# Kernel optimization log

Measured on AMD Instinct MI355X. Metric: run time of the kernel, lower is better.

The kernel has to match this reference:

```python
import jax, jax.numpy as jnp
import numpy as np

B, T, D = 4, 4096, 1024
EPS = 1e-5  # FusedRMSNormSwishGate default eps


def setup_inputs() -> dict:
    key = jax.random.key(0)
    ks = jax.random.split(key, 6)
    s = 1.0 / np.sqrt(D)
    return {
        "x": jax.random.normal(ks[0], (B, T, D), jnp.float32),
        "Wi": jax.random.normal(ks[1], (D, D), jnp.float32) * s,
        "Wf": jax.random.normal(ks[2], (D, D), jnp.float32) * s,
        "Wg": jax.random.normal(ks[3], (D, D), jnp.float32) * s,
        "Wo": jax.random.normal(ks[4], (D, D), jnp.float32) * s,
        "norm_w": jnp.ones((D,), jnp.float32),
    }


def _hgrn_scan(f, i):
    # h_t = f_t * h_{t-1} + i_t  (elementwise gated linear recurrence)
    # associative combine: (f1,i1) o (f2,i2) = (f1*f2, i1*f2 + i2)
    def combine(a, b):
        fa, ia = a
        fb, ib = b
        return fa * fb, ia * fb + ib

    _, h = jax.lax.associative_scan(combine, (f, i), axis=1)
    return h


def reference(x, Wi, Wf, Wg, Wo, norm_w):
    # projections
    i = x @ Wi.T                                  # [B,T,D]
    f = jax.nn.sigmoid(x @ Wf.T)                  # forget gate in (0,1)
    # swiglu(i, 1-f): silu on the value, gated by the input gate (1-f)
    inp = jax.nn.silu(i) * (1.0 - f)
    # hierarchically-gated linear recurrence (chunk/parallel scan form)
    h = _hgrn_scan(f, inp)                        # [B,T,D]
    # RMSNorm(h) * swish(g) output gate
    g = x @ Wg.T
    rms = h * jax.lax.rsqrt(jnp.mean(h * h, axis=-1, keepdims=True) + EPS)
    o = (rms * norm_w) * (g * jax.nn.sigmoid(g))
    return o @ Wo.T
```

## Files before the change

kernel.cpp:

```cpp
#include <hip/hip_runtime.h>
#include <hip/hip_bf16.h>

typedef unsigned short u16;
using bf16x8 = __bf16 __attribute__((ext_vector_type(8)));
using f32x4  = float  __attribute__((ext_vector_type(4)));

#define BB 4
#define TT 4096
#define DD 1024
#define MROWS (BB*TT)
#define CT 64
#define NC (TT/CT)

__device__ __forceinline__ float sigm(float x) { return 1.0f / (1.0f + __expf(-x)); }
__device__ __forceinline__ u16 f2bf(float f) {
    __hip_bfloat16 h = __float2bfloat16(f);
    return *reinterpret_cast<u16*>(&h);
}
__device__ __forceinline__ float bf2f(u16 u) { return __uint_as_float(((unsigned)u) << 16); }

__device__ __forceinline__ void async_cp16(const u16* g, u16* l) {
    __builtin_amdgcn_global_load_lds(
        (const __attribute__((address_space(1))) unsigned int*)g,
        (__attribute__((address_space(3))) unsigned int*)l, 16, 0, 0);
}

__global__ __launch_bounds__(256) void conv_x_kernel(const float* __restrict__ s,
                                                     u16* __restrict__ d) {
    size_t i = (size_t)blockIdx.x * 256 + threadIdx.x;
    float4 v = *(const float4*)(s + i * 4);
    ushort4 u;
    u.x = f2bf(v.x); u.y = f2bf(v.y); u.z = f2bf(v.z); u.w = f2bf(v.w);
    *(ushort4*)(d + i * 4) = u;
}

__global__ __launch_bounds__(256) void conv_w4_kernel(const float* __restrict__ w0,
                                                      const float* __restrict__ w1,
                                                      const float* __restrict__ w2,
                                                      const float* __restrict__ w3,
                                                      u16* __restrict__ dst) {
    int i = blockIdx.x * 256 + threadIdx.x;
    int sel = i >> 18;
    int off = i & 262143;
    const float* s = (sel == 0) ? w0 : (sel == 1) ? w1 : (sel == 2) ? w2 : w3;
    float4 v = *(const float4*)(s + (size_t)off * 4);
    ushort4 u;
    u.x = f2bf(v.x); u.y = f2bf(v.y); u.z = f2bf(v.z); u.w = f2bf(v.w);
    *(ushort4*)(dst + ((size_t)sel << 20) + (size_t)off * 4) = u;
}

#define G_BM 256
#define G_BN 256
#define G_BK 64

#define READ_A(dst, MH)                                                         \
  { const u16* Ab = &As[(p * 2 + (MH)) << 13];                                  \
    _Pragma("unroll") for (int kk = 0; kk < 2; kk++) {                          \
      const int gsw = (((kk * 4 + lq) ^ lr7) << 3);                             \
      _Pragma("unroll") for (int f = 0; f < 4; f++)                             \
        dst[f][kk] = *(const bf16x8*)(Ab + (wm * 64 + f * 16 + lr) * 64 + gsw); \
    } }
#define READ_B(dst, NH)                                                         \
  { const u16* Bb = &Bs[(p * 2 + (NH)) << 13];                                  \
    _Pragma("unroll") for (int kk = 0; kk < 2; kk++) {                          \
      const int gsw = (((kk * 4 + lq) ^ lr7) << 3);                             \
      _Pragma("unroll") for (int j = 0; j < 2; j++)                             \
        dst[j][kk] = *(const bf16x8*)(Bb + (wn * 32 + j * 16 + lr) * 64 + gsw); \
    } }
#define MFMA16(AV, BV, MH, NH)                                                  \
  { _Pragma("unroll") for (int kk = 0; kk < 2; kk++)                            \
    _Pragma("unroll") for (int f = 0; f < 4; f++)                               \
    _Pragma("unroll") for (int j = 0; j < 2; j++)                               \
      acc[(MH)*4+f][(NH)*2+j] = __builtin_amdgcn_mfma_f32_16x16x32_bf16(        \
          AV[f][kk], BV[j][kk], acc[(MH)*4+f][(NH)*2+j], 0, 0, 0); }
#define SYNC_PRE()                                                              \
  do { __builtin_amdgcn_s_barrier();                                            \
       asm volatile("s_waitcnt lgkmcnt(0)" ::: "memory");                       \
       __builtin_amdgcn_s_setprio(1); } while (0)
#define SYNC_POST()                                                             \
  do { __builtin_amdgcn_s_setprio(0);                                           \
       __builtin_amdgcn_s_barrier(); } while (0)

template <typename OutT>
__global__ __launch_bounds__(512, 2)
void gemm256(const u16* __restrict__ Ag, const u16* __restrict__ Bg, int K,
             OutT* __restrict__ P0, OutT* __restrict__ P1, OutT* __restrict__ P2) {
    __shared__ u16 As[32768];
    __shared__ u16 Bs[32768];

    const int tid  = threadIdx.x;
    const int lane = tid & 63;
    const int wid  = tid >> 6;
    const int wm   = wid >> 2;
    const int wn   = wid & 3;
    const int lr   = lane & 15;
    const int lq   = lane >> 4;
    const int lr7  = lr & 7;

    const long bM  = (long)blockIdx.y * G_BM;
    const long bN0 = (long)blockIdx.x * G_BN;
    const int  KT  = K >> 6;

    auto stageA = [&](int cc, int h) {
#pragma unroll
        for (int l = 0; l < 2; l++) {
            const int G  = l * 512 + tid;
            const int rl = G >> 3;
            const int gk = (G & 7) ^ (rl & 7);
            const int r  = (rl & 63) + h * 64 + ((rl >> 6) << 7);
            async_cp16(Ag + (bM + r) * K + cc * 64 + gk * 8,
                       &As[(((cc & 1) * 2 + h) << 13) + G * 8]);
        }
    };
    auto stageB = [&](int cc, int h) {
#pragma unroll
        for (int l = 0; l < 2; l++) {
            const int G  = l * 512 + tid;
            const int rl = G >> 3;
            const int gk = (G & 7) ^ (rl & 7);
            const int r  = (rl & 31) + h * 32 + ((rl >> 5) << 6);
            async_cp16(Bg + (bN0 + r) * K + cc * 64 + gk * 8,
                       &Bs[(((cc & 1) * 2 + h) << 13) + G * 8]);
        }
    };

    const f32x4 zero = {0.f, 0.f, 0.f, 0.f};
    f32x4 acc[8][4];
#pragma unroll
    for (int i = 0; i < 8; i++)
#pragma unroll
        for (int j = 0; j < 4; j++) acc[i][j] = zero;

    stageA(0, 0); stageB(0, 0); stageA(0, 1); stageB(0, 1);
    if (KT > 1) {
        stageA(1, 0); stageB(1, 0);
        asm volatile("s_waitcnt vmcnt(4)" ::: "memory");
    } else {
        asm volatile("s_waitcnt vmcnt(0)" ::: "memory");
    }
    __builtin_amdgcn_s_barrier();

    for (int c = 0; c < KT; ++c) {
        const int  p  = c & 1;
        const bool s1 = (c + 1 < KT);
        const bool s2 = (c + 2 < KT);
        bf16x8 av0[4][2], av1[4][2], bv0[2][2], bv1[2][2];
        READ_A(av0, 0); READ_B(bv0, 0);
        if (s1) stageA(c + 1, 1);
        SYNC_PRE(); MFMA16(av0, bv0, 0, 0); SYNC_POST();
        READ_B(bv1, 1);
        if (s1) stageB(c + 1, 1);
        SYNC_PRE(); MFMA16(av0, bv1, 0, 1); SYNC_POST();
        READ_A(av1, 1);
        if (s2) stageA(c + 2, 0);
        SYNC_PRE(); MFMA16(av1, bv0, 1, 0); SYNC_POST();
        if (s2) {
            stageB(c + 2, 0);
            asm volatile("s_waitcnt vmcnt(4)" ::: "memory");
        } else if (s1) {
            asm volatile("s_waitcnt vmcnt(0)" ::: "memory");
        }
        SYNC_PRE(); MFMA16(av1, bv1, 1, 1); SYNC_POST();
    }

    const int pl = (int)(bN0 >> 10);
    OutT* P = (pl == 0) ? P0 : ((pl == 1) ? P1 : P2);
    const int cn = (int)(bN0 & 1023);
#pragma unroll
    for (int i = 0; i < 8; i++) {
        const long m0 = bM + wm * 128 + i * 16 + lq * 4;
#pragma unroll
        for (int j = 0; j < 4; j++) {
            const int n = cn + wn * 64 + j * 16 + lr;
#pragma unroll
            for (int r = 0; r < 4; r++) {
                if constexpr (sizeof(OutT) == 2)
                    P[(m0 + r) * 1024 + n] = f2bf(acc[i][j][r]);
                else
                    P[(m0 + r) * 1024 + n] = acc[i][j][r];
            }
        }
    }
}

__global__ __launch_bounds__(256) void scan_pass1(const u16* __restrict__ ip,
                                                  const u16* __restrict__ fp,
                                                  float* __restrict__ Fc,
                                                  float* __restrict__ Ic) {
    const int tid = blockIdx.x * 256 + threadIdx.x;
    const int d4  = tid & 255;
    const int c   = (tid >> 8) & (NC - 1);
    const int b   = tid >> 14;
    size_t base = ((size_t)(b * TT + c * CT) << 10) + (size_t)d4 * 4;
    float F[4] = {1.f, 1.f, 1.f, 1.f};
    float I[4] = {0.f, 0.f, 0.f, 0.f};
#pragma unroll 8
    for (int t = 0; t < CT; t++) {
        ushort4 fu = *(const ushort4*)(fp + base);
        ushort4 iu = *(const ushort4*)(ip + base);
        base += DD;
        const u16 fa[4] = {fu.x, fu.y, fu.z, fu.w};
        const u16 ia[4] = {iu.x, iu.y, iu.z, iu.w};
#pragma unroll
        for (int j = 0; j < 4; j++) {
            float f  = sigm(bf2f(fa[j]));
            float iv = bf2f(ia[j]);
            float v  = iv * sigm(iv) * (1.f - f);
            I[j] = fmaf(f, I[j], v);
            F[j] *= f;
        }
    }
    const size_t o = (((size_t)(b * NC + c)) << 10) + (size_t)d4 * 4;
    float4 vF = {F[0], F[1], F[2], F[3]};
    float4 vI = {I[0], I[1], I[2], I[3]};
    *(float4*)(Fc + o) = vF;
    *(float4*)(Ic + o) = vI;
}

__global__ __launch_bounds__(256) void scan_pass2(const float* __restrict__ Fc,
                                                  const float* __restrict__ Ic,
                                                  float* __restrict__ Hin) {
    const int gtid = blockIdx.x * 256 + threadIdx.x;
    const int lane = gtid & 63;
    const int w    = gtid >> 6;
    const int b    = w >> 10;
    const int d    = w & 1023;
    const int idx  = ((b * NC + lane) << 10) + d;
    float F = Fc[idx];
    float I = Ic[idx];
#pragma unroll
    for (int s = 1; s < 64; s <<= 1) {
        float Fp = __shfl_up(F, s, 64);
        float Ip = __shfl_up(I, s, 64);
        if (lane >= s) {
            I = fmaf(Ip, F, I);
            F *= Fp;
        }
    }
    float Hex = __shfl_up(I, 1, 64);
    if (lane == 0) Hex = 0.f;
    Hin[idx] = Hex;
}

__global__ __launch_bounds__(256) void scan_pass3(const u16* __restrict__ ip,
                                                  const u16* __restrict__ fp,
                                                  const float* __restrict__ Hin,
                                                  u16* __restrict__ hout) {
    const int tid = blockIdx.x * 256 + threadIdx.x;
    const int d4  = tid & 255;
    const int c   = (tid >> 8) & (NC - 1);
    const int b   = tid >> 14;
    size_t base = ((size_t)(b * TT + c * CT) << 10) + (size_t)d4 * 4;
    const size_t o = (((size_t)(b * NC + c)) << 10) + (size_t)d4 * 4;
    float4 hv = *(const float4*)(Hin + o);
    float h[4] = {hv.x, hv.y, hv.z, hv.w};
#pragma unroll 8
    for (int t = 0; t < CT; t++) {
        ushort4 fu = *(const ushort4*)(fp + base);
        ushort4 iu = *(const ushort4*)(ip + base);
        const u16 fa[4] = {fu.x, fu.y, fu.z, fu.w};
        const u16 ia[4] = {iu.x, iu.y, iu.z, iu.w};
        ushort4 ou;
        u16 oa[4];
#pragma unroll
        for (int j = 0; j < 4; j++) {
            float f  = sigm(bf2f(fa[j]));
            float iv = bf2f(ia[j]);
            float v  = iv * sigm(iv) * (1.f - f);
            h[j] = fmaf(f, h[j], v);
            oa[j] = f2bf(h[j]);
        }
        ou.x = oa[0]; ou.y = oa[1]; ou.z = oa[2]; ou.w = oa[3];
        *(ushort4*)(hout + base) = ou;
        base += DD;
    }
}

__global__ __launch_bounds__(256) void rmsnorm_gate(const u16* hin,
                                                    const u16* __restrict__ g,
                                                    const float* __restrict__ w,
                                                    u16* oout) {
    const int row = blockIdx.x;
    const int t = threadIdx.x;
    const size_t base = ((size_t)row << 10) + t * 4;
    ushort4 hu = *(const ushort4*)(hin + base);
    float h0 = bf2f(hu.x), h1 = bf2f(hu.y), h2 = bf2f(hu.z), h3 = bf2f(hu.w);
    float ss = h0 * h0 + h1 * h1 + h2 * h2 + h3 * h3;
#pragma unroll
    for (int o = 32; o > 0; o >>= 1) ss += __shfl_down(ss, o);
    __shared__ float red[4];
    if ((t & 63) == 0) red[t >> 6] = ss;
    __syncthreads();
    const float tot = red[0] + red[1] + red[2] + red[3];
    const float rms = rsqrtf(tot * (1.f / 1024.f) + 1e-5f);
    ushort4 gu = *(const ushort4*)(g + base);
    float g0 = bf2f(gu.x), g1 = bf2f(gu.y), g2 = bf2f(gu.z), g3 = bf2f(gu.w);
    float4 wv = *(const float4*)(w + (size_t)t * 4);
    ushort4 ou;
    ou.x = f2bf(h0 * rms * wv.x * g0 * sigm(g0));
    ou.y = f2bf(h1 * rms * wv.y * g1 * sigm(g1));
    ou.z = f2bf(h2 * rms * wv.z * g2 * sigm(g2));
    ou.w = f2bf(h3 * rms * wv.w * g3 * sigm(g3));
    *(ushort4*)(oout + base) = ou;
}

extern "C" void kernel_launch(void* const* d_in, const int* in_sizes, int n_in,
                              void* d_out, int out_size, void* d_ws, size_t ws_size,
                              hipStream_t stream) {
    const float* x  = (const float*)d_in[0];
    const float* Wi = (const float*)d_in[1];
    const float* Wf = (const float*)d_in[2];
    const float* Wg = (const float*)d_in[3];
    const float* Wo = (const float*)d_in[4];
    const float* nw = (const float*)d_in[5];
    float* out = (float*)d_out;

    const size_t MB = 1ull << 20;
    char* ws = (char*)d_ws;
    u16*   xo  = (u16*)(ws);
    u16*   Wb  = (u16*)(ws + 32 * MB);
    u16*   Pi  = (u16*)(ws + 40 * MB);
    u16*   Pf  = (u16*)(ws + 72 * MB);
    float* Fc  = (float*)(ws + 104 * MB);
    float* Ic  = Fc + BB * NC * DD;
    float* Hin = Ic + BB * NC * DD;
    u16*   g   = (u16*)d_out;

    conv_x_kernel<<<16384, 256, 0, stream>>>(x, xo);
    conv_w4_kernel<<<4096, 256, 0, stream>>>(Wi, Wf, Wg, Wo, Wb);
    gemm256<u16><<<dim3(12, 64), 512, 0, stream>>>(xo, Wb, 1024, Pi, Pf, g);
    scan_pass1<<<256, 256, 0, stream>>>(Pi, Pf, Fc, Ic);
    scan_pass2<<<1024, 256, 0, stream>>>(Fc, Ic, Hin);
    scan_pass3<<<256, 256, 0, stream>>>(Pi, Pf, Hin, xo);
    rmsnorm_gate<<<16384, 256, 0, stream>>>(xo, g, nw, xo);
    gemm256<float><<<dim3(4, 64), 512, 0, stream>>>(xo, Wb + 3ull * 1024 * 1024, 1024,
                                                    out, out, out);
}
```

Baseline: 382.2 us.

## Use inline-asm LDS reads in big GEMM and smaller-tile GEMM for output projection

The fused QKV-style 256x256 GEMM now reads LDS through inline ds_read_b128 with immediate offsets and adds a sched_barrier so the compiler cannot reorder them around the sync points. The final output projection switches to a new, simpler 128x128-tile kernel with 256 threads, launched on 1024 blocks instead of 256. The aim is to cut LDS address arithmetic and to fill more CUs on the small final GEMM. The trade-off is that the new kernel is single-buffered and synchronous, with no load/compute overlap.

```diff
diff --git a/kernel.cpp b/kernel.cpp
--- a/kernel.cpp
+++ b/kernel.cpp
@@ -49,33 +49,118 @@
     *(ushort4*)(dst + ((size_t)sel << 20) + (size_t)off * 4) = u;
 }
 
-#define G_BM 256
-#define G_BN 256
-#define G_BK 64
-
-#define READ_A(dst, MH)                                                         \
-  { const u16* Ab = &As[(p * 2 + (MH)) << 13];                                  \
-    _Pragma("unroll") for (int kk = 0; kk < 2; kk++) {                          \
-      const int gsw = (((kk * 4 + lq) ^ lr7) << 3);                             \
-      _Pragma("unroll") for (int f = 0; f < 4; f++)                             \
-        dst[f][kk] = *(const bf16x8*)(Ab + (wm * 64 + f * 16 + lr) * 64 + gsw); \
-    } }
-#define READ_B(dst, NH)                                                         \
-  { const u16* Bb = &Bs[(p * 2 + (NH)) << 13];                                  \
-    _Pragma("unroll") for (int kk = 0; kk < 2; kk++) {                          \
-      const int gsw = (((kk * 4 + lq) ^ lr7) << 3);                             \
-      _Pragma("unroll") for (int j = 0; j < 2; j++)                             \
-        dst[j][kk] = *(const bf16x8*)(Bb + (wn * 32 + j * 16 + lr) * 64 + gsw); \
-    } }
+#define BM 128
+#define BN 128
+#define BK 64
+
+template <typename OutT>
+__global__ __launch_bounds__(256, 2)
+void gemm_bf16_bt(const u16* __restrict__ Ag, const u16* __restrict__ Bg, int K,
+                  OutT* __restrict__ P0, OutT* __restrict__ P1, OutT* __restrict__ P2) {
+    __shared__ u16 As[BM * BK];
+    __shared__ u16 Bs[BN * BK];
+
+    const int tid  = threadIdx.x;
+    const int lane = tid & 63;
+    const int wid  = tid >> 6;
+    const int wm   = wid >> 1;
+    const int wn   = wid & 1;
+    const int lr   = lane & 15;
+    const int lq   = lane >> 4;
+
+    const long bM  = (long)blockIdx.y * BM;
+    const long bN0 = (long)blockIdx.x * BN;
+
+    const f32x4 zero = {0.f, 0.f, 0.f, 0.f};
+    f32x4 acc[4][4];
+#pragma unroll
+    for (int i = 0; i < 4; i++)
+#pragma unroll
+        for (int j = 0; j < 4; j++) acc[i][j] = zero;
+
+    for (int kt = 0; kt < K; kt += BK) {
+        __syncthreads();
+#pragma unroll
+        for (int j = 0; j < 4; j++) {
+            const int G  = j * 256 + tid;
+            const int m  = G >> 3;
+            const int p  = G & 7;
+            const int gk = p ^ (m & 7);
+            async_cp16(Ag + (bM + m) * K + kt + gk * 8, &As[G * 8]);
+            async_cp16(Bg + (bN0 + m) * K + kt + gk * 8, &Bs[G * 8]);
+        }
+        __syncthreads();
+#pragma unroll
+        for (int kk = 0; kk < BK / 32; kk++) {
+            bf16x8 av[4], bv[4];
+#pragma unroll
+            for (int f = 0; f < 4; f++) {
+                const int am = wm * 64 + f * 16 + lr;
+                const int ag = (kk * 4 + lq) ^ (am & 7);
+                av[f] = *(const bf16x8*)(&As[am * 64 + ag * 8]);
+                const int bn = wn * 64 + f * 16 + lr;
+                const int bg = (kk * 4 + lq) ^ (bn & 7);
+                bv[f] = *(const bf16x8*)(&Bs[bn * 64 + bg * 8]);
+            }
+#pragma unroll
+            for (int i = 0; i < 4; i++)
+#pragma unroll
+                for (int j = 0; j < 4; j++)
+                    acc[i][j] = __builtin_amdgcn_mfma_f32_16x16x32_bf16(av[i], bv[j],
+                                                                        acc[i][j], 0, 0, 0);
+        }
+    }
+
+    const int pl = (int)(bN0 >> 10);
+    OutT* P = (pl == 0) ? P0 : ((pl == 1) ? P1 : P2);
+    const int cn = (int)(bN0 & 1023);
+#pragma unroll
+    for (int i = 0; i < 4; i++) {
+        const long m0 = bM + wm * 64 + i * 16 + lq * 4;
+#pragma unroll
+        for (int j = 0; j < 4; j++) {
+            const int n = cn + wn * 64 + j * 16 + lr;
+#pragma unroll
+            for (int r = 0; r < 4; r++) {
+                if constexpr (sizeof(OutT) == 2)
+                    P[(m0 + r) * 1024 + n] = f2bf(acc[i][j][r]);
+                else
+                    P[(m0 + r) * 1024 + n] = acc[i][j][r];
+            }
+        }
+    }
+}
+
+#define DSR(dst, a, OFF) \
+    asm volatile("ds_read_b128 %0, %1 offset:" OFF : "=v"(dst) : "v"(a))
+
+#define READ_A_ASM(dst, MH) { \
+    const unsigned a0 = asB + (unsigned)(p << 15) + ((MH) << 14) \
+                        + (wm * 64 + lr) * 128 + ((lq ^ lr7) << 4); \
+    const unsigned a1 = a0 ^ 64; \
+    DSR(dst[0][0], a0, "0");    DSR(dst[1][0], a0, "2048"); \
+    DSR(dst[2][0], a0, "4096"); DSR(dst[3][0], a0, "6144"); \
+    DSR(dst[0][1], a1, "0");    DSR(dst[1][1], a1, "2048"); \
+    DSR(dst[2][1], a1, "4096"); DSR(dst[3][1], a1, "6144"); }
+
+#define READ_B_ASM(dst, NH) { \
+    const unsigned b0 = bsB + (unsigned)(p << 15) + ((NH) << 14) \
+                        + (wn * 32 + lr) * 128 + ((lq ^ lr7) << 4); \
+    const unsigned b1 = b0 ^ 64; \
+    DSR(dst[0][0], b0, "0");    DSR(dst[1][0], b0, "2048"); \
+    DSR(dst[0][1], b1, "0");    DSR(dst[1][1], b1, "2048"); }
+
 #define MFMA16(AV, BV, MH, NH)                                                  \
   { _Pragma("unroll") for (int kk = 0; kk < 2; kk++)                            \
     _Pragma("unroll") for (int f = 0; f < 4; f++)                               \
     _Pragma("unroll") for (int j = 0; j < 2; j++)                               \
       acc[(MH)*4+f][(NH)*2+j] = __builtin_amdgcn_mfma_f32_16x16x32_bf16(        \
           AV[f][kk], BV[j][kk], acc[(MH)*4+f][(NH)*2+j], 0, 0, 0); }
+
 #define SYNC_PRE()                                                              \
   do { __builtin_amdgcn_s_barrier();                                            \
        asm volatile("s_waitcnt lgkmcnt(0)" ::: "memory");                       \
+       __builtin_amdgcn_sched_barrier(0);                                       \
        __builtin_amdgcn_s_setprio(1); } while (0)
 #define SYNC_POST()                                                             \
   do { __builtin_amdgcn_s_setprio(0);                                           \
@@ -83,8 +168,8 @@
 
 template <typename OutT>
 __global__ __launch_bounds__(512, 2)
-void gemm256(const u16* __restrict__ Ag, const u16* __restrict__ Bg, int K,
-             OutT* __restrict__ P0, OutT* __restrict__ P1, OutT* __restrict__ P2) {
+void gemm256a(const u16* __restrict__ Ag, const u16* __restrict__ Bg, int K,
+              OutT* __restrict__ P0, OutT* __restrict__ P1, OutT* __restrict__ P2) {
     __shared__ u16 As[32768];
     __shared__ u16 Bs[32768];
 
@@ -97,8 +182,11 @@
     const int lq   = lane >> 4;
     const int lr7  = lr & 7;
 
-    const long bM  = (long)blockIdx.y * G_BM;
-    const long bN0 = (long)blockIdx.x * G_BN;
+    const unsigned asB = (unsigned)(uintptr_t)&As[0];
+    const unsigned bsB = (unsigned)(uintptr_t)&Bs[0];
+
+    const long bM  = (long)blockIdx.y * 256;
+    const long bN0 = (long)blockIdx.x * 256;
     const int  KT  = K >> 6;
 
     auto stageA = [&](int cc, int h) {
@@ -145,13 +233,13 @@
         const bool s1 = (c + 1 < KT);
         const bool s2 = (c + 2 < KT);
         bf16x8 av0[4][2], av1[4][2], bv0[2][2], bv1[2][2];
-        READ_A(av0, 0); READ_B(bv0, 0);
+        READ_A_ASM(av0, 0); READ_B_ASM(bv0, 0);
         if (s1) stageA(c + 1, 1);
         SYNC_PRE(); MFMA16(av0, bv0, 0, 0); SYNC_POST();
-        READ_B(bv1, 1);
+        READ_B_ASM(bv1, 1);
         if (s1) stageB(c + 1, 1);
         SYNC_PRE(); MFMA16(av0, bv1, 0, 1); SYNC_POST();
-        READ_A(av1, 1);
+        READ_A_ASM(av1, 1);
         if (s2) stageA(c + 2, 0);
         SYNC_PRE(); MFMA16(av1, bv0, 1, 0); SYNC_POST();
         if (s2) {
@@ -328,11 +416,11 @@
 
     conv_x_kernel<<<16384, 256, 0, stream>>>(x, xo);
     conv_w4_kernel<<<4096, 256, 0, stream>>>(Wi, Wf, Wg, Wo, Wb);
-    gemm256<u16><<<dim3(12, 64), 512, 0, stream>>>(xo, Wb, 1024, Pi, Pf, g);
+    gemm256a<u16><<<dim3(12, 64), 512, 0, stream>>>(xo, Wb, 1024, Pi, Pf, g);
     scan_pass1<<<256, 256, 0, stream>>>(Pi, Pf, Fc, Ic);
     scan_pass2<<<1024, 256, 0, stream>>>(Fc, Ic, Hin);
     scan_pass3<<<256, 256, 0, stream>>>(Pi, Pf, Hin, xo);
     rmsnorm_gate<<<16384, 256, 0, stream>>>(xo, g, nw, xo);
-    gemm256<float><<<dim3(4, 64), 512, 0, stream>>>(xo, Wb + 3ull * 1024 * 1024, 1024,
-                                                    out, out, out);
-}
+    gemm_bf16_bt<float><<<dim3(8, 128), 256, 0, stream>>>(xo, Wb + 3ull * 1024 * 1024, 1024,
+                                                          out, out, out);
+}
```

Measured after the change: 389.5 us. About the same (+1.9%).
